# Kernel optimization log

Hardware: AMD Instinct MI355X
Metric: run time of the kernel (lower is better)

## Reference

```python
import math
import jax, jax.numpy as jnp
import numpy as np

N = 2_000_000
L_MAX = 8


def setup_inputs() -> dict:
    key = jax.random.key(0)
    k1, k2 = jax.random.split(key)
    # cos_theta uniform in (-1, 1), phi uniform in (-pi, pi)
    cos_theta = jax.random.uniform(k1, (N,), dtype=jnp.float32, minval=-0.999, maxval=0.999)
    phi = jax.random.uniform(k2, (N,), dtype=jnp.float32, minval=-math.pi, maxval=math.pi)
    return {"l_max": L_MAX, "cos_theta": cos_theta, "phi": phi}


def _real_spherical_harmonics(l_max, cos_theta, phi):
    """Real spherical harmonics Y_{l,m}, flattened as [N, (l_max+1)^2].

    Uses the standard associated-Legendre recurrences (no Condon-Shortley
    phase) and the orthonormal real-SH normalization
      K(l,m) = sqrt((2l+1)/(4pi) * (l-m)!/(l+m)!).
    """
    ct = cos_theta
    st = jnp.sqrt(jnp.maximum(1.0 - ct * ct, 0.0))  # sin(theta) >= 0

    # Associated Legendre P_l^m(ct) via recurrence; small fixed (l, m) loop.
    P = {(0, 0): jnp.ones_like(ct)}
    for m in range(1, l_max + 1):
        P[(m, m)] = P[(m - 1, m - 1)] * st * (2 * m - 1)          # P_m^m
    for m in range(0, l_max):
        P[(m + 1, m)] = ct * (2 * m + 1) * P[(m, m)]              # P_{m+1}^m
    for m in range(0, l_max + 1):
        for l in range(m + 2, l_max + 1):
            P[(l, m)] = ((2 * l - 1) * ct * P[(l - 1, m)]
                         - (l + m - 1) * P[(l - 2, m)]) / (l - m)

    cols = []
    sqrt2 = math.sqrt(2.0)
    for l in range(l_max + 1):
        for m in range(-l, l + 1):
            am = abs(m)
            k = math.sqrt((2 * l + 1) / (4.0 * math.pi)
                          * math.factorial(l - am) / math.factorial(l + am))
            if m < 0:
                cols.append((sqrt2 * k) * P[(l, am)] * jnp.sin(am * phi))
            elif m == 0:
                cols.append(k * P[(l, 0)])
            else:
                cols.append((sqrt2 * k) * P[(l, m)] * jnp.cos(m * phi))
    return jnp.stack(cols, axis=1)  # [N, (l_max+1)^2]


def reference(l_max, cos_theta, phi):
    return _real_spherical_harmonics(int(l_max), cos_theta, phi)
```

## Files before the change

### kernel.cpp

```cpp
#include <hip/hip_runtime.h>
#include <math.h>


namespace {

constexpr double csqrt(double x) {
    double g = x > 1.0 ? x : 1.0;
    for (int i = 0; i < 200; ++i) g = 0.5 * (g + x / g);
    return g;
}
constexpr double cfact(int n) {
    double r = 1.0;
    for (int i = 2; i <= n; ++i) r *= (double)i;
    return r;
}
constexpr double PI_D = 3.14159265358979323846264338327950288;

constexpr float coefv(int l, int m) {
    const int am = m < 0 ? -m : m;
    const double k = csqrt((2.0 * l + 1.0) / (4.0 * PI_D) * cfact(l - am) / cfact(l + am));
    const double s2 = 1.4142135623730950488016887242097;
    return (float)((m == 0 ? 1.0 : s2) * k);
}

struct CoefTab { float v[81]; };
constexpr CoefTab make_tab() {
    CoefTab t{};
    for (int l = 0; l <= 8; ++l)
        for (int m = -l; m <= l; ++m)
            t.v[l * l + l + m] = coefv(l, m);
    return t;
}
constexpr CoefTab COEF = make_tab();

}

#define LMAX 8
#define NCOL 81
#define PTS_PER_BLOCK 64
#define FLOATS_PER_TILE (PTS_PER_BLOCK * NCOL)
#define VEC4_PER_TILE (FLOATS_PER_TILE / 4)

__global__ __launch_bounds__(PTS_PER_BLOCK)
void sh_kernel(const float* __restrict__ ct_in, const float* __restrict__ phi_in,
               float* __restrict__ out, int n) {
    __shared__ __align__(16) float lds[FLOATS_PER_TILE];
    const int lane = threadIdx.x;
    const long long tile = blockIdx.x;
    const long long idx = tile * PTS_PER_BLOCK + lane;

    if (idx < n) {
        const float ct = ct_in[idx];
        const float phi = phi_in[idx];
        const float st = sqrtf(fmaxf(1.0f - ct * ct, 0.0f));
        float sp, cp;
        __sincosf(phi, &sp, &cp);

        float* row = lds + lane * NCOL;

        float pmm = 1.0f;
        float cm = 1.0f;
        float sm = 0.0f;
#pragma unroll
        for (int m = 0; m <= LMAX; ++m) {
            if (m > 0) {
                pmm *= st * (float)(2 * m - 1);
                const float cn = cm * cp - sm * sp;
                const float sn = sm * cp + cm * sp;
                cm = cn; sm = sn;
            }
            {
                const int b = m * m + m;
                if (m == 0) {
                    row[b] = COEF.v[b] * pmm;
                } else {
                    row[b + m] = COEF.v[b + m] * pmm * cm;
                    row[b - m] = COEF.v[b - m] * pmm * sm;
                }
            }
            if (m < LMAX) {
                float p_prev = pmm;
                float p_cur = ct * (float)(2 * m + 1) * pmm;
                {
                    const int l = m + 1;
                    const int b = l * l + l;
                    if (m == 0) {
                        row[b] = COEF.v[b] * p_cur;
                    } else {
                        row[b + m] = COEF.v[b + m] * p_cur * cm;
                        row[b - m] = COEF.v[b - m] * p_cur * sm;
                    }
                }
#pragma unroll
                for (int l = m + 2; l <= LMAX; ++l) {
                    const float inv = 1.0f / (float)(l - m);
                    const float p_next = ((float)(2 * l - 1) * ct * p_cur
                                          - (float)(l + m - 1) * p_prev) * inv;
                    p_prev = p_cur; p_cur = p_next;
                    const int b = l * l + l;
                    if (m == 0) {
                        row[b] = COEF.v[b] * p_cur;
                    } else {
                        row[b + m] = COEF.v[b + m] * p_cur * cm;
                        row[b - m] = COEF.v[b - m] * p_cur * sm;
                    }
                }
            }
        }
    }
    __syncthreads();

    float4* __restrict__ outv = (float4*)(out + tile * (long long)FLOATS_PER_TILE);
    const float4* lv = (const float4*)lds;
    const long long tile_base_f4 = tile * (long long)VEC4_PER_TILE;
    const long long total_f4 = ((long long)n * NCOL) / 4;
#pragma unroll
    for (int j = 0; j < 20; ++j) {
        const int e = j * 64 + lane;
        if (tile_base_f4 + e < total_f4) outv[e] = lv[e];
    }
    {
        const int e = 20 * 64 + lane;
        if (lane < 16 && tile_base_f4 + e < total_f4) outv[e] = lv[e];
    }
}

extern "C" void kernel_launch(void* const* d_in, const int* in_sizes, int n_in,
                              void* d_out, int out_size, void* d_ws, size_t ws_size,
                              hipStream_t stream) {
    const float* ct  = (const float*)d_in[1];
    const float* phi = (const float*)d_in[2];
    float* out = (float*)d_out;
    const int n = in_sizes[1];
    const int blocks = (n + PTS_PER_BLOCK - 1) / PTS_PER_BLOCK;
    sh_kernel<<<blocks, PTS_PER_BLOCK, 0, stream>>>(ct, phi, out, n);
}
```

Baseline: 646.9 us.

## Use persistent grid-stride blocks with next-tile input prefetch and wave barriers

Replaces the one-tile-per-block launch with a persistent grid of about 1792 single-wave blocks that loop over tiles in grid-stride order. The next tile's inputs are loaded before the current tile is stored, `__syncthreads` becomes a wave barrier since each block is one wavefront, and full tiles take an unguarded store path. The aim is to cut block launch overhead and per-element bounds checks and to hide input load latency. The fixed grid size may underfill the GPU or limit how many stores are in flight on a bandwidth-bound write.

```diff
diff --git a/kernel.cpp b/kernel.cpp
--- a/kernel.cpp
+++ b/kernel.cpp
@@ -37,27 +37,33 @@
 
 #define LMAX 8
 #define NCOL 81
-#define PTS_PER_BLOCK 64
-#define FLOATS_PER_TILE (PTS_PER_BLOCK * NCOL)
-#define VEC4_PER_TILE (FLOATS_PER_TILE / 4)
+#define PTS 64
+#define TILE_FLOATS (PTS * NCOL)
+#define TILE_F4 (TILE_FLOATS / 4)
 
-__global__ __launch_bounds__(PTS_PER_BLOCK)
+__global__ __launch_bounds__(PTS)
 void sh_kernel(const float* __restrict__ ct_in, const float* __restrict__ phi_in,
                float* __restrict__ out, int n) {
-    __shared__ __align__(16) float lds[FLOATS_PER_TILE];
+    __shared__ __align__(16) float lds[TILE_FLOATS];
     const int lane = threadIdx.x;
-    const long long tile = blockIdx.x;
-    const long long idx = tile * PTS_PER_BLOCK + lane;
+    const int ntiles = (n + PTS - 1) / PTS;
+    const long long total_f4 = ((long long)n * NCOL) / 4;
+    const long long stride = gridDim.x;
 
-    if (idx < n) {
-        const float ct = ct_in[idx];
-        const float phi = phi_in[idx];
+    long long tile = blockIdx.x;
+    if (tile >= ntiles) return;
+
+    long long cidx = tile * PTS + lane;
+    if (cidx >= n) cidx = (long long)n - 1;
+    float ct  = ct_in[cidx];
+    float phi = phi_in[cidx];
+
+    while (tile < ntiles) {
         const float st = sqrtf(fmaxf(1.0f - ct * ct, 0.0f));
         float sp, cp;
         __sincosf(phi, &sp, &cp);
 
         float* row = lds + lane * NCOL;
-
         float pmm = 1.0f;
         float cm = 1.0f;
         float sm = 0.0f;
@@ -107,21 +113,34 @@
                 }
             }
         }
-    }
-    __syncthreads();
 
-    float4* __restrict__ outv = (float4*)(out + tile * (long long)FLOATS_PER_TILE);
-    const float4* lv = (const float4*)lds;
-    const long long tile_base_f4 = tile * (long long)VEC4_PER_TILE;
-    const long long total_f4 = ((long long)n * NCOL) / 4;
+        const long long ntile = tile + stride;
+        {
+            long long nidx = ntile * PTS + lane;
+            if (nidx >= n) nidx = (long long)n - 1;
+            ct  = ct_in[nidx];
+            phi = phi_in[nidx];
+        }
+
+        __builtin_amdgcn_wave_barrier();
+
+        float4* __restrict__ outv = (float4*)out + tile * (long long)TILE_F4;
+        const float4* lv = (const float4*)lds;
+        const long long base = tile * (long long)TILE_F4;
+        if (base + TILE_F4 <= total_f4) {
 #pragma unroll
-    for (int j = 0; j < 20; ++j) {
-        const int e = j * 64 + lane;
-        if (tile_base_f4 + e < total_f4) outv[e] = lv[e];
-    }
-    {
-        const int e = 20 * 64 + lane;
-        if (lane < 16 && tile_base_f4 + e < total_f4) outv[e] = lv[e];
+            for (int j = 0; j < 20; ++j) outv[j * 64 + lane] = lv[j * 64 + lane];
+            if (lane < 16) outv[20 * 64 + lane] = lv[20 * 64 + lane];
+        } else {
+#pragma unroll
+            for (int j = 0; j < 21; ++j) {
+                const int e = j * 64 + lane;
+                if (e < TILE_F4 && base + e < total_f4) outv[e] = lv[e];
+            }
+        }
+
+        __builtin_amdgcn_wave_barrier();
+        tile = ntile;
     }
 }
 
@@ -132,6 +151,8 @@
     const float* phi = (const float*)d_in[2];
     float* out = (float*)d_out;
     const int n = in_sizes[1];
-    const int blocks = (n + PTS_PER_BLOCK - 1) / PTS_PER_BLOCK;
-    sh_kernel<<<blocks, PTS_PER_BLOCK, 0, stream>>>(ct, phi, out, n);
+    const int ntiles = (n + PTS - 1) / PTS;
+    int blocks = 7 * 256;
+    if (blocks > ntiles) blocks = ntiles;
+    sh_kernel<<<blocks, PTS, 0, stream>>>(ct, phi, out, n);
 }
```

Result: no change. 656.0 us (+1.4%).
